# Kernel optimization log

Hardware: AMD Instinct MI355X
Metric: run time of the kernel (lower is better)

Reference implementation:

```python
import jax, jax.numpy as jnp
import numpy as np

N_NODES = 100000
N_EDGES = 3200000
IN_DIM = 4
BIG = 32
HID = 2
BN_EPS = 1e-5


def _lin_init(key, fan_in, fan_out):
    k1, k2 = jax.random.split(key)
    bound = 1.0 / np.sqrt(fan_in)
    W = jax.random.uniform(k1, (fan_in, fan_out), minval=-bound, maxval=bound, dtype=jnp.float32)
    b = jax.random.uniform(k2, (fan_out,), minval=-bound, maxval=bound, dtype=jnp.float32)
    return W, b


def setup_inputs() -> dict:
    key = jax.random.key(0)
    ks = jax.random.split(key, 12)
    x = jax.random.normal(ks[0], (N_NODES, IN_DIM), dtype=jnp.float32)
    edge_index = jax.random.randint(ks[1], (2, N_EDGES), 0, N_NODES, dtype=jnp.int32)
    eps_noise = jax.random.normal(ks[2], (N_NODES, HID), dtype=jnp.float32)
    # batchnorm affine params
    bn_gamma = jnp.ones((IN_DIM,), jnp.float32)
    bn_beta = jnp.zeros((IN_DIM,), jnp.float32)
    # encoder EdgeConv MLP: 2*IN_DIM -> BIG -> BIG
    eW1, eb1 = _lin_init(ks[3], 2 * IN_DIM, BIG)
    eW2, eb2 = _lin_init(ks[4], BIG, BIG)
    # mu / logvar heads
    mW, mb = _lin_init(ks[5], BIG, HID)
    vW, vb = _lin_init(ks[6], BIG, HID)
    # decoder EdgeConv MLP: 2*HID -> BIG -> BIG -> IN_DIM
    dW1, db1 = _lin_init(ks[7], 2 * HID, BIG)
    dW2, db2 = _lin_init(ks[8], BIG, BIG)
    dW3, db3 = _lin_init(ks[9], BIG, IN_DIM)
    return dict(x=x, edge_index=edge_index, eps_noise=eps_noise,
                bn_gamma=bn_gamma, bn_beta=bn_beta,
                eW1=eW1, eb1=eb1, eW2=eW2, eb2=eb2,
                mW=mW, mb=mb, vW=vW, vb=vb,
                dW1=dW1, db1=db1, dW2=dW2, db2=db2, dW3=dW3, db3=db3)


def _segment_mean(msgs, tgt, n):
    s = jax.ops.segment_sum(msgs, tgt, num_segments=n)
    c = jax.ops.segment_sum(jnp.ones((msgs.shape[0],), msgs.dtype), tgt, num_segments=n)
    return s / jnp.maximum(c, 1.0)[:, None]


def _edge_conv(x, edge_index, mlp):
    # PyG EdgeConv: h_i = mean_{j->i} nn([x_i, x_j - x_i])
    src, tgt = edge_index[0], edge_index[1]
    x_i = x[tgt]                      # [E, F]
    x_j = x[src]                      # [E, F]
    feat = jnp.concatenate([x_i, x_j - x_i], axis=-1)  # [E, 2F]
    msg = mlp(feat)                   # [E, F_out]
    return _segment_mean(msg, tgt, x.shape[0])


def reference(x, edge_index, eps_noise, bn_gamma, bn_beta,
              eW1, eb1, eW2, eb2, mW, mb, vW, vb,
              dW1, db1, dW2, db2, dW3, db3):
    # BatchNorm1d (training mode: batch statistics, biased variance)
    mean = jnp.mean(x, axis=0)
    var = jnp.var(x, axis=0)
    xn = (x - mean) * jax.lax.rsqrt(var + BN_EPS) * bn_gamma + bn_beta

    enc_mlp = lambda f: jax.nn.relu(jax.nn.relu(f @ eW1 + eb1) @ eW2 + eb2)
    h = _edge_conv(xn, edge_index, enc_mlp)           # [N, BIG]

    mu = h @ mW + mb                                  # [N, HID]
    log_var = h @ vW + vb                             # [N, HID]
    z = mu + eps_noise * jnp.exp(0.5 * log_var)       # reparameterize

    dec_mlp = lambda f: jax.nn.relu(jax.nn.relu(f @ dW1 + db1) @ dW2 + db2) @ dW3 + db3
    out = _edge_conv(z, edge_index, dec_mlp)          # [N, IN_DIM]
    return out, mu, log_var
```

## Files before the change

### kernel.cpp

```cpp
#include <hip/hip_runtime.h>
#include <math.h>

#define N_NODES 100000
#define N_EDGES 3200000
#define NBLK_EDGE ((N_EDGES + 255) / 256)
#define NBLK_NODE ((N_NODES + 255) / 256)

#define NB 64
#define NBUCK ((N_NODES + NB - 1) / NB)
#define NSLICE 256
#define SLICE (N_EDGES / NSLICE)
#define P2 2048

typedef _Float16 h2f16 __attribute__((ext_vector_type(2)));
typedef __fp16 f16x8 __attribute__((ext_vector_type(8)));
typedef float f32x4 __attribute__((ext_vector_type(4)));
typedef unsigned u32x4 __attribute__((ext_vector_type(4)));

#define PK_ENC_A2 0
#define PK_DEC_A2 512
#define PK_ENC_W1 1024
#define PK_DEC_W1 1152
#define PK_ENC_H 1216
#define PK_DEC_H 1280
#define PK_TOTAL 1344

__device__ __forceinline__ h2f16 mkh2(float a, float b) {
  h2f16 h;
  h.x = (_Float16)a;
  h.y = (_Float16)b;
  return h;
}
__device__ __forceinline__ float fdot2(h2f16 a, h2f16 b, float c) {
  return __builtin_amdgcn_fdot2(a, b, c, false);
}
__device__ __forceinline__ h2f16 pk(float a, float b) {
  auto r = __builtin_amdgcn_cvt_pkrtz(a, b);
  return __builtin_bit_cast(h2f16, r);
}
__device__ __forceinline__ unsigned h2u(h2f16 h) {
  return __builtin_bit_cast(unsigned, h);
}
__device__ __forceinline__ f32x4 mfma16(f16x8 a, f16x8 b, f32x4 c) {
  return __builtin_amdgcn_mfma_f32_16x16x32_f16(a, b, c, 0, 0, 0);
}

__global__ __launch_bounds__(256) void pack_weights(
    const float* __restrict__ eW1, const float* __restrict__ eW2,
    const float* __restrict__ mW, const float* __restrict__ vW,
    const float* __restrict__ dW1, const float* __restrict__ dW2,
    const float* __restrict__ dW3, h2f16* __restrict__ wpk) {
  int t = threadIdx.x;
  for (int i = t; i < 512; i += 256) {
    int tl = i >> 8, rest = i & 255, lane = rest >> 2, p = rest & 3;
    int q = lane >> 4, c = lane & 15;
    int k0 = q * 8 + 2 * p, out = 16 * tl + c;
    wpk[PK_ENC_A2 + i] = mkh2(eW2[k0 * 32 + out], eW2[(k0 + 1) * 32 + out]);
    wpk[PK_DEC_A2 + i] = mkh2(dW2[k0 * 32 + out], dW2[(k0 + 1) * 32 + out]);
  }
  for (int i = t; i < 128; i += 256) {
    int q = i >> 5, j = (i >> 2) & 7, kp = i & 3;
    wpk[PK_ENC_W1 + i] =
        mkh2(eW1[(2 * kp) * 32 + q * 8 + j], eW1[(2 * kp + 1) * 32 + q * 8 + j]);
  }
  for (int i = t; i < 64; i += 256) {
    int q = i >> 4, j = (i >> 1) & 7, kp = i & 1;
    wpk[PK_DEC_W1 + i] =
        mkh2(dW1[(2 * kp) * 32 + q * 8 + j], dW1[(2 * kp + 1) * 32 + q * 8 + j]);
  }
  for (int i = t; i < 64; i += 256) {
    int q = i >> 4, r = (i >> 2) & 3, h = i & 3;
    int o0 = 4 * q + r, o1 = 16 + 4 * q + r;
    float w0 = (h < 2) ? mW[o0 * 2 + h] : vW[o0 * 2 + (h - 2)];
    float w1 = (h < 2) ? mW[o1 * 2 + h] : vW[o1 * 2 + (h - 2)];
    wpk[PK_ENC_H + i] = mkh2(w0, w1);
    wpk[PK_DEC_H + i] = mkh2(dW3[o0 * 4 + h], dW3[o1 * 4 + h]);
  }
}

__global__ void bn_reduce(const float4* __restrict__ x, float* __restrict__ bns) {
  float s0 = 0, s1 = 0, s2 = 0, s3 = 0, q0 = 0, q1 = 0, q2 = 0, q3 = 0;
  for (int i = blockIdx.x * blockDim.x + threadIdx.x; i < N_NODES;
       i += gridDim.x * blockDim.x) {
    float4 v = x[i];
    s0 += v.x; s1 += v.y; s2 += v.z; s3 += v.w;
    q0 += v.x * v.x; q1 += v.y * v.y; q2 += v.z * v.z; q3 += v.w * v.w;
  }
#pragma unroll
  for (int o = 32; o; o >>= 1) {
    s0 += __shfl_down(s0, o); s1 += __shfl_down(s1, o);
    s2 += __shfl_down(s2, o); s3 += __shfl_down(s3, o);
    q0 += __shfl_down(q0, o); q1 += __shfl_down(q1, o);
    q2 += __shfl_down(q2, o); q3 += __shfl_down(q3, o);
  }
  __shared__ float red[4][8];
  int w = threadIdx.x >> 6;
  if ((threadIdx.x & 63) == 0) {
    red[w][0] = s0; red[w][1] = s1; red[w][2] = s2; red[w][3] = s3;
    red[w][4] = q0; red[w][5] = q1; red[w][6] = q2; red[w][7] = q3;
  }
  __syncthreads();
  if (threadIdx.x < 8) {
    float acc = red[0][threadIdx.x] + red[1][threadIdx.x] +
                red[2][threadIdx.x] + red[3][threadIdx.x];
    atomicAdd(&bns[threadIdx.x], acc);
  }
}

__global__ void bn_final(const float* __restrict__ bns,
                         const float* __restrict__ gamma,
                         const float* __restrict__ beta,
                         float* __restrict__ ab) {
  int d = threadIdx.x;
  if (d < 4) {
    float mean = bns[d] * (1.0f / N_NODES);
    float var = bns[4 + d] * (1.0f / N_NODES) - mean * mean;
    float a = gamma[d] * rsqrtf(var + 1e-5f);
    ab[d] = a;
    ab[4 + d] = beta[d] - mean * a;
  }
}

__global__ __launch_bounds__(256) void edge_hist(const int* __restrict__ tgt,
                                                 unsigned* __restrict__ hist) {
  __shared__ unsigned h[NBUCK];
  for (int i = threadIdx.x; i < NBUCK; i += 256) h[i] = 0;
  __syncthreads();
  int e0 = blockIdx.x * SLICE;
  for (int i = threadIdx.x; i < SLICE; i += 256)
    atomicAdd(&h[((unsigned)tgt[e0 + i]) >> 6], 1u);
  __syncthreads();
  for (int i = threadIdx.x; i < NBUCK; i += 256)
    hist[(size_t)blockIdx.x * NBUCK + i] = h[i];
}

__global__ __launch_bounds__(256) void bucket_tot(const unsigned* __restrict__ hist,
                                                  unsigned* __restrict__ tot) {
  int k = blockIdx.x * 256 + threadIdx.x;
  if (k >= NBUCK) return;
  unsigned s = 0;
#pragma unroll 8
  for (int b = 0; b < NSLICE; ++b) s += hist[(size_t)b * NBUCK + k];
  tot[k] = s;
}

__global__ __launch_bounds__(1024) void bucket_start(const unsigned* __restrict__ tot,
                                                     unsigned* __restrict__ start) {
  __shared__ unsigned sa[P2], sb[P2];
  for (int k = threadIdx.x; k < P2; k += 1024)
    sa[k] = (k < NBUCK) ? tot[k] : 0u;
  __syncthreads();
  unsigned *srcp = sa, *dstp = sb;
  for (int off = 1; off < P2; off <<= 1) {
    for (int k = threadIdx.x; k < P2; k += 1024)
      dstp[k] = srcp[k] + (k >= off ? srcp[k - off] : 0u);
    __syncthreads();
    unsigned* t = srcp; srcp = dstp; dstp = t;
  }
  for (int k = threadIdx.x; k <= NBUCK; k += 1024)
    start[k] = (k == 0) ? 0u : srcp[k - 1];
}

__global__ __launch_bounds__(256) void bucket_bases(unsigned* __restrict__ hist,
                                                    const unsigned* __restrict__ start) {
  int wv = threadIdx.x >> 6, lane = threadIdx.x & 63;
  int k = blockIdx.x * 4 + wv;
  if (k >= NBUCK) return;
  unsigned v0 = hist[(size_t)(4 * lane + 0) * NBUCK + k];
  unsigned v1 = hist[(size_t)(4 * lane + 1) * NBUCK + k];
  unsigned v2 = hist[(size_t)(4 * lane + 2) * NBUCK + k];
  unsigned v3 = hist[(size_t)(4 * lane + 3) * NBUCK + k];
  unsigned p1 = v0, p2 = v0 + v1, p3 = v0 + v1 + v2;
  unsigned s = p3 + v3;
  unsigned incl = s;
#pragma unroll
  for (int off = 1; off < 64; off <<= 1) {
    unsigned t = __shfl_up(incl, off);
    incl += (lane >= off) ? t : 0u;
  }
  unsigned base = start[k] + (incl - s);
  hist[(size_t)(4 * lane + 0) * NBUCK + k] = base;
  hist[(size_t)(4 * lane + 1) * NBUCK + k] = base + p1;
  hist[(size_t)(4 * lane + 2) * NBUCK + k] = base + p2;
  hist[(size_t)(4 * lane + 3) * NBUCK + k] = base + p3;
}

__global__ __launch_bounds__(256) void edge_place(
    const int* __restrict__ src, const int* __restrict__ tgt,
    const unsigned* __restrict__ hist, const unsigned* __restrict__ start,
    unsigned* __restrict__ payload) {
  __shared__ unsigned stage[SLICE];
  __shared__ unsigned offA[NBUCK];
  __shared__ unsigned A2[NBUCK];
  int s = blockIdx.x, tid = threadIdx.x;
  for (int k = tid; k < NBUCK; k += 256) {
    unsigned gb = hist[(size_t)s * NBUCK + k];
    unsigned nb = (s == NSLICE - 1) ? start[k + 1]
                                    : hist[(size_t)(s + 1) * NBUCK + k];
    offA[k] = gb;
    A2[k] = nb - gb;
  }
  __syncthreads();
  for (int d = 1; d < NBUCK; d <<= 1) {
    unsigned tmp[7];
    int m = 0;
    for (int k = tid; k < NBUCK; k += 256, ++m)
      tmp[m] = (k >= d) ? A2[k - d] : 0u;
    __syncthreads();
    m = 0;
    for (int k = tid; k < NBUCK; k += 256, ++m) A2[k] += tmp[m];
    __syncthreads();
  }
  {
    unsigned tmp[7];
    int m = 0;
    for (int k = tid; k < NBUCK; k += 256, ++m)
      tmp[m] = (k == 0) ? 0u : A2[k - 1];
    __syncthreads();
    m = 0;
    for (int k = tid; k < NBUCK; k += 256, ++m) {
      offA[k] -= tmp[m];
      A2[k] = tmp[m];
    }
    __syncthreads();
  }
  int e0 = s * SLICE;
  for (int i = tid; i < SLICE; i += 256) {
    unsigned t = (unsigned)tgt[e0 + i];
    unsigned sr = (unsigned)src[e0 + i];
    unsigned b = t >> 6;
    unsigned lp = atomicAdd(&A2[b], 1u);
    stage[lp] = sr | ((t & 63u) << 17);
  }
  __syncthreads();
  for (int b = tid; b < NBUCK; b += 256) {
    unsigned beg = (b == 0) ? 0u : A2[b - 1];
    unsigned end = A2[b];
    unsigned go = offA[b];
    for (unsigned i = beg; i < end; ++i) payload[go + i] = stage[i];
  }
}

__global__ __launch_bounds__(256) void enc_bucket(
    const float4* __restrict__ x, const unsigned* __restrict__ payload,
    const unsigned* __restrict__ start, const float* __restrict__ ab,
    const float* __restrict__ eb1, const float* __restrict__ eb2,
    const h2f16* __restrict__ wpk, float2* __restrict__ mpart,
    float2* __restrict__ vpart, float* __restrict__ cpart) {
  __shared__ float aM0[NB], aM1[NB], aV0[NB], aV1[NB], aC[NB];
  __shared__ float4 xt[NB];
  int k = blockIdx.x, node0 = k * NB, h = blockIdx.y;
  int tid = threadIdx.x, w = tid >> 6, lane = tid & 63;
  int q = lane >> 4, c = lane & 15;
  if (tid < NB) {
    int n = node0 + tid;
    aM0[tid] = 0; aM1[tid] = 0; aV0[tid] = 0; aV1[tid] = 0; aC[tid] = 0;
    xt[tid] = x[n < N_NODES ? n : 0];
  }
  __syncthreads();
  float a0 = ab[0], a1 = ab[1], a2 = ab[2], a3 = ab[3];
  float b0 = ab[4], b1 = ab[5], b2 = ab[6], b3 = ab[7];
  const u32x4* a2b = (const u32x4*)(wpk + PK_ENC_A2);
  f16x8 A0 = __builtin_bit_cast(f16x8, a2b[lane]);
  f16x8 A1 = __builtin_bit_cast(f16x8, a2b[64 + lane]);
  h2f16 w1e[32];
#pragma unroll
  for (int i = 0; i < 32; ++i) w1e[i] = wpk[PK_ENC_W1 + q * 32 + i];
  h2f16 hw[16];
#pragma unroll
  for (int i = 0; i < 16; ++i) hw[i] = wpk[PK_ENC_H + q * 16 + i];
  float eb1v[8];
#pragma unroll
  for (int j = 0; j < 8; ++j) eb1v[j] = eb1[q * 8 + j];
  float e2a[4], e2b[4];
#pragma unroll
  for (int r = 0; r < 4; ++r) {
    e2a[r] = eb2[4 * q + r];
    e2b[r] = eb2[16 + 4 * q + r];
  }
  unsigned s0v = start[k], s1v = start[k + 1];
  unsigned len = s1v - s0v, halfv = (len + 1) >> 1;
  unsigned lo = s0v + (h ? halfv : 0u);
  unsigned hi = h ? s1v : (s0v + halfv);
  for (unsigned base = lo + (unsigned)w * 32; base < hi; base += 128) {
    unsigned eA = base + (unsigned)c;
    unsigned eB = eA + 16;
    unsigned pA = payload[eA < hi ? eA : hi - 1];
    unsigned pB = payload[eB < hi ? eB : hi - 1];
    int siA = (int)(pA & 0x1FFFFu), siB = (int)(pB & 0x1FFFFu);
    int ltiA = (int)(pA >> 17), ltiB = (int)(pB >> 17);
    float4 xjA = x[siA];
    float4 xjB = x[siB];
    float4 xiA = xt[ltiA];
    float4 xiB = xt[ltiB];
    h2f16 fA0 = pk(fmaf(a0, xiA.x, b0), fmaf(a1, xiA.y, b1));
    h2f16 fA1 = pk(fmaf(a2, xiA.z, b2), fmaf(a3, xiA.w, b3));
    h2f16 fA2 = pk(a0 * (xjA.x - xiA.x), a1 * (xjA.y - xiA.y));
    h2f16 fA3 = pk(a2 * (xjA.z - xiA.z), a3 * (xjA.w - xiA.w));
    h2f16 fB0 = pk(fmaf(a0, xiB.x, b0), fmaf(a1, xiB.y, b1));
    h2f16 fB1 = pk(fmaf(a2, xiB.z, b2), fmaf(a3, xiB.w, b3));
    h2f16 fB2 = pk(a0 * (xjB.x - xiB.x), a1 * (xjB.y - xiB.y));
    h2f16 fB3 = pk(a2 * (xjB.z - xiB.z), a3 * (xjB.w - xiB.w));
    float rA[8], rB[8];
#pragma unroll
    for (int j = 0; j < 8; ++j) {
      float uA = eb1v[j], uB = eb1v[j];
      uA = fdot2(fA0, w1e[4 * j + 0], uA);
      uB = fdot2(fB0, w1e[4 * j + 0], uB);
      uA = fdot2(fA1, w1e[4 * j + 1], uA);
      uB = fdot2(fB1, w1e[4 * j + 1], uB);
      uA = fdot2(fA2, w1e[4 * j + 2], uA);
      uB = fdot2(fB2, w1e[4 * j + 2], uB);
      uA = fdot2(fA3, w1e[4 * j + 3], uA);
      uB = fdot2(fB3, w1e[4 * j + 3], uB);
      rA[j] = fmaxf(uA, 0.0f);
      rB[j] = fmaxf(uB, 0.0f);
    }
    u32x4 buA, buB;
    buA[0] = h2u(pk(rA[0], rA[1])); buA[1] = h2u(pk(rA[2], rA[3]));
    buA[2] = h2u(pk(rA[4], rA[5])); buA[3] = h2u(pk(rA[6], rA[7]));
    buB[0] = h2u(pk(rB[0], rB[1])); buB[1] = h2u(pk(rB[2], rB[3]));
    buB[2] = h2u(pk(rB[4], rB[5])); buB[3] = h2u(pk(rB[6], rB[7]));
    f16x8 BA = __builtin_bit_cast(f16x8, buA);
    f16x8 BB = __builtin_bit_cast(f16x8, buB);
    f32x4 zf = {0.f, 0.f, 0.f, 0.f};
    f32x4 C0A = mfma16(A0, BA, zf), C1A = mfma16(A1, BA, zf);
    f32x4 C0B = mfma16(A0, BB, zf), C1B = mfma16(A1, BB, zf);
    float m0A = 0, m1A = 0, v0A = 0, v1A = 0;
    float m0B = 0, m1B = 0, v0B = 0, v1B = 0;
#pragma unroll
    for (int rr = 0; rr < 4; ++rr) {
      h2f16 hA = pk(fmaxf(C0A[rr] + e2a[rr], 0.0f),
                    fmaxf(C1A[rr] + e2b[rr], 0.0f));
      h2f16 hB = pk(fmaxf(C0B[rr] + e2a[rr], 0.0f),
                    fmaxf(C1B[rr] + e2b[rr], 0.0f));
      m0A = fdot2(hA, hw[4 * rr + 0], m0A);
      m0B = fdot2(hB, hw[4 * rr + 0], m0B);
      m1A = fdot2(hA, hw[4 * rr + 1], m1A);
      m1B = fdot2(hB, hw[4 * rr + 1], m1B);
      v0A = fdot2(hA, hw[4 * rr + 2], v0A);
      v0B = fdot2(hB, hw[4 * rr + 2], v0B);
      v1A = fdot2(hA, hw[4 * rr + 3], v1A);
      v1B = fdot2(hB, hw[4 * rr + 3], v1B);
    }
    m0A += __shfl_xor(m0A, 16); m0A += __shfl_xor(m0A, 32);
    m1A += __shfl_xor(m1A, 16); m1A += __shfl_xor(m1A, 32);
    v0A += __shfl_xor(v0A, 16); v0A += __shfl_xor(v0A, 32);
    v1A += __shfl_xor(v1A, 16); v1A += __shfl_xor(v1A, 32);
    m0B += __shfl_xor(m0B, 16); m0B += __shfl_xor(m0B, 32);
    m1B += __shfl_xor(m1B, 16); m1B += __shfl_xor(m1B, 32);
    v0B += __shfl_xor(v0B, 16); v0B += __shfl_xor(v0B, 32);
    v1B += __shfl_xor(v1B, 16); v1B += __shfl_xor(v1B, 32);
    if (lane < 16) {
      if (eA < hi) {
        atomicAdd(&aM0[ltiA], m0A);
        atomicAdd(&aM1[ltiA], m1A);
        atomicAdd(&aV0[ltiA], v0A);
        atomicAdd(&aV1[ltiA], v1A);
        atomicAdd(&aC[ltiA], 1.0f);
      }
      if (eB < hi) {
        atomicAdd(&aM0[ltiB], m0B);
        atomicAdd(&aM1[ltiB], m1B);
        atomicAdd(&aV0[ltiB], v0B);
        atomicAdd(&aV1[ltiB], v1B);
        atomicAdd(&aC[ltiB], 1.0f);
      }
    }
  }
  __syncthreads();
  if (tid < NB) {
    int n = node0 + tid;
    if (n < N_NODES) {
      mpart[(size_t)h * N_NODES + n] = make_float2(aM0[tid], aM1[tid]);
      vpart[(size_t)h * N_NODES + n] = make_float2(aV0[tid], aV1[tid]);
      cpart[(size_t)h * N_NODES + n] = aC[tid];
    }
  }
}

__global__ __launch_bounds__(256) void node_mid(
    const float2* __restrict__ mpart, const float2* __restrict__ vpart,
    const float* __restrict__ cpart, const float* __restrict__ eps2,
    const float* __restrict__ mbias, const float* __restrict__ vbias,
    float* __restrict__ z, float* __restrict__ cntC,
    float2* __restrict__ muOut, float2* __restrict__ lvOut) {
  int n = blockIdx.x * 256 + threadIdx.x;
  if (n >= N_NODES) return;
  float2 ma = mpart[n], mb2 = mpart[N_NODES + n];
  float2 va = vpart[n], vb2 = vpart[N_NODES + n];
  float cc = cpart[n] + cpart[N_NODES + n];
  float inv = 1.0f / fmaxf(cc, 1.0f);
  float mu0 = fmaf(ma.x + mb2.x, inv, mbias[0]);
  float mu1 = fmaf(ma.y + mb2.y, inv, mbias[1]);
  float lv0 = fmaf(va.x + vb2.x, inv, vbias[0]);
  float lv1 = fmaf(va.y + vb2.y, inv, vbias[1]);
  cntC[n] = cc;
  muOut[n] = make_float2(mu0, mu1);
  lvOut[n] = make_float2(lv0, lv1);
  z[2 * n + 0] = fmaf(eps2[2 * n + 0], expf(0.5f * lv0), mu0);
  z[2 * n + 1] = fmaf(eps2[2 * n + 1], expf(0.5f * lv1), mu1);
}

__global__ __launch_bounds__(256) void dec_bucket(
    const float2* __restrict__ z, const unsigned* __restrict__ payload,
    const unsigned* __restrict__ start, const float* __restrict__ db1,
    const float* __restrict__ db2, const float* __restrict__ db3,
    const h2f16* __restrict__ wpk, float4* __restrict__ opart) {
  __shared__ float aO0[NB], aO1[NB], aO2[NB], aO3[NB];
  __shared__ float2 zt[NB];
  int k = blockIdx.x, node0 = k * NB, h = blockIdx.y;
  int tid = threadIdx.x, w = tid >> 6, lane = tid & 63;
  int q = lane >> 4, c = lane & 15;
  if (tid < NB) {
    int n = node0 + tid;
    aO0[tid] = 0; aO1[tid] = 0; aO2[tid] = 0; aO3[tid] = 0;
    zt[tid] = z[n < N_NODES ? n : 0];
  }
  __syncthreads();
  const u32x4* a2b = (const u32x4*)(wpk + PK_DEC_A2);
  f16x8 A0 = __builtin_bit_cast(f16x8, a2b[lane]);
  f16x8 A1 = __builtin_bit_cast(f16x8, a2b[64 + lane]);
  h2f16 w1d[16];
#pragma unroll
  for (int i = 0; i < 16; ++i) w1d[i] = wpk[PK_DEC_W1 + q * 16 + i];
  h2f16 hw[16];
#pragma unroll
  for (int i = 0; i < 16; ++i) hw[i] = wpk[PK_DEC_H + q * 16 + i];
  float db1v[8];
#pragma unroll
  for (int j = 0; j < 8; ++j) db1v[j] = db1[q * 8 + j];
  float d2a[4], d2b[4];
#pragma unroll
  for (int r = 0; r < 4; ++r) {
    d2a[r] = db2[4 * q + r];
    d2b[r] = db2[16 + 4 * q + r];
  }
  float b3_0 = db3[0], b3_1 = db3[1], b3_2 = db3[2], b3_3 = db3[3];
  unsigned s0v = start[k], s1v = start[k + 1];
  unsigned len = s1v - s0v, halfv = (len + 1) >> 1;
  unsigned lo = s0v + (h ? halfv : 0u);
  unsigned hi = h ? s1v : (s0v + halfv);
  for (unsigned base = lo + (unsigned)w * 32; base < hi; base += 128) {
    unsigned eA = base + (unsigned)c;
    unsigned eB = eA + 16;
    unsigned pA = payload[eA < hi ? eA : hi - 1];
    unsigned pB = payload[eB < hi ? eB : hi - 1];
    int siA = (int)(pA & 0x1FFFFu), siB = (int)(pB & 0x1FFFFu);
    int ltiA = (int)(pA >> 17), ltiB = (int)(pB >> 17);
    float2 zjA = z[siA];
    float2 zjB = z[siB];
    float2 ziA = zt[ltiA];
    float2 ziB = zt[ltiB];
    h2f16 fA0 = pk(ziA.x, ziA.y);
    h2f16 fA1 = pk(zjA.x - ziA.x, zjA.y - ziA.y);
    h2f16 fB0 = pk(ziB.x, ziB.y);
    h2f16 fB1 = pk(zjB.x - ziB.x, zjB.y - ziB.y);
    float rA[8], rB[8];
#pragma unroll
    for (int j = 0; j < 8; ++j) {
      float uA = db1v[j], uB = db1v[j];
      uA = fdot2(fA0, w1d[2 * j + 0], uA);
      uB = fdot2(fB0, w1d[2 * j + 0], uB);
      uA = fdot2(fA1, w1d[2 * j + 1], uA);
      uB = fdot2(fB1, w1d[2 * j + 1], uB);
      rA[j] = fmaxf(uA, 0.0f);
      rB[j] = fmaxf(uB, 0.0f);
    }
    u32x4 buA, buB;
    buA[0] = h2u(pk(rA[0], rA[1])); buA[1] = h2u(pk(rA[2], rA[3]));
    buA[2] = h2u(pk(rA[4], rA[5])); buA[3] = h2u(pk(rA[6], rA[7]));
    buB[0] = h2u(pk(rB[0], rB[1])); buB[1] = h2u(pk(rB[2], rB[3]));
    buB[2] = h2u(pk(rB[4], rB[5])); buB[3] = h2u(pk(rB[6], rB[7]));
    f16x8 BA = __builtin_bit_cast(f16x8, buA);
    f16x8 BB = __builtin_bit_cast(f16x8, buB);
    f32x4 zf = {0.f, 0.f, 0.f, 0.f};
    f32x4 C0A = mfma16(A0, BA, zf), C1A = mfma16(A1, BA, zf);
    f32x4 C0B = mfma16(A0, BB, zf), C1B = mfma16(A1, BB, zf);
    float o0A = 0, o1A = 0, o2A = 0, o3A = 0;
    float o0B = 0, o1B = 0, o2B = 0, o3B = 0;
#pragma unroll
    for (int rr = 0; rr < 4; ++rr) {
      h2f16 hA = pk(fmaxf(C0A[rr] + d2a[rr], 0.0f),
                    fmaxf(C1A[rr] + d2b[rr], 0.0f));
      h2f16 hB = pk(fmaxf(C0B[rr] + d2a[rr], 0.0f),
                    fmaxf(C1B[rr] + d2b[rr], 0.0f));
      o0A = fdot2(hA, hw[4 * rr + 0], o0A);
      o0B = fdot2(hB, hw[4 * rr + 0], o0B);
      o1A = fdot2(hA, hw[4 * rr + 1], o1A);
      o1B = fdot2(hB, hw[4 * rr + 1], o1B);
      o2A = fdot2(hA, hw[4 * rr + 2], o2A);
      o2B = fdot2(hB, hw[4 * rr + 2], o2B);
      o3A = fdot2(hA, hw[4 * rr + 3], o3A);
      o3B = fdot2(hB, hw[4 * rr + 3], o3B);
    }
    o0A += __shfl_xor(o0A, 16); o0A += __shfl_xor(o0A, 32);
    o1A += __shfl_xor(o1A, 16); o1A += __shfl_xor(o1A, 32);
    o2A += __shfl_xor(o2A, 16); o2A += __shfl_xor(o2A, 32);
    o3A += __shfl_xor(o3A, 16); o3A += __shfl_xor(o3A, 32);
    o0B += __shfl_xor(o0B, 16); o0B += __shfl_xor(o0B, 32);
    o1B += __shfl_xor(o1B, 16); o1B += __shfl_xor(o1B, 32);
    o2B += __shfl_xor(o2B, 16); o2B += __shfl_xor(o2B, 32);
    o3B += __shfl_xor(o3B, 16); o3B += __shfl_xor(o3B, 32);
    if (lane < 16) {
      if (eA < hi) {
        atomicAdd(&aO0[ltiA], o0A + b3_0);
        atomicAdd(&aO1[ltiA], o1A + b3_1);
        atomicAdd(&aO2[ltiA], o2A + b3_2);
        atomicAdd(&aO3[ltiA], o3A + b3_3);
      }
      if (eB < hi) {
        atomicAdd(&aO0[ltiB], o0B + b3_0);
        atomicAdd(&aO1[ltiB], o1B + b3_1);
        atomicAdd(&aO2[ltiB], o2B + b3_2);
        atomicAdd(&aO3[ltiB], o3B + b3_3);
      }
    }
  }
  __syncthreads();
  if (tid < NB) {
    int n = node0 + tid;
    if (n < N_NODES)
      opart[(size_t)h * N_NODES + n] =
          make_float4(aO0[tid], aO1[tid], aO2[tid], aO3[tid]);
  }
}

__global__ __launch_bounds__(256) void node_final(
    const float4* __restrict__ opart, const float* __restrict__ cntC,
    float4* __restrict__ outp) {
  int n = blockIdx.x * 256 + threadIdx.x;
  if (n >= N_NODES) return;
  float4 a = opart[n], b = opart[N_NODES + n];
  float inv = 1.0f / fmaxf(cntC[n], 1.0f);
  outp[n] = make_float4((a.x + b.x) * inv, (a.y + b.y) * inv,
                        (a.z + b.z) * inv, (a.w + b.w) * inv);
}

__device__ __forceinline__ void atomAddF(float* p, float v) {
  unsafeAtomicAdd(p, v);
}

__global__ __launch_bounds__(256) void enc_edge_fb(
    const float4* __restrict__ x, const int* __restrict__ esrc,
    const int* __restrict__ etgt, const float* __restrict__ ab,
    const float* __restrict__ eW1, const float* __restrict__ eb1,
    const float* __restrict__ eW2, const float* __restrict__ eb2,
    const float* __restrict__ mW, const float* __restrict__ vW,
    float* __restrict__ msum, float* __restrict__ vsum,
    float* __restrict__ cnt) {
  int e = blockIdx.x * 256 + threadIdx.x;
  if (e >= N_EDGES) return;
  int si = esrc[e], ti = etgt[e];
  float4 xi = x[ti];
  float4 xj = x[si];
  float a0 = ab[0], a1 = ab[1], a2 = ab[2], a3 = ab[3];
  float b0 = ab[4], b1 = ab[5], b2 = ab[6], b3 = ab[7];
  float feat[8];
  feat[0] = fmaf(a0, xi.x, b0);
  feat[1] = fmaf(a1, xi.y, b1);
  feat[2] = fmaf(a2, xi.z, b2);
  feat[3] = fmaf(a3, xi.w, b3);
  feat[4] = a0 * (xj.x - xi.x);
  feat[5] = a1 * (xj.y - xi.y);
  feat[6] = a2 * (xj.z - xi.z);
  feat[7] = a3 * (xj.w - xi.w);
  float h1[32];
#pragma unroll 8
  for (int j = 0; j < 32; ++j) {
    float acc = eb1[j];
#pragma unroll
    for (int kk = 0; kk < 8; ++kk) acc = fmaf(feat[kk], eW1[kk * 32 + j], acc);
    h1[j] = fmaxf(acc, 0.0f);
  }
  float m0 = 0, m1 = 0, v0 = 0, v1 = 0;
#pragma unroll 4
  for (int j = 0; j < 32; ++j) {
    float acc = eb2[j];
#pragma unroll
    for (int kk = 0; kk < 32; ++kk) acc = fmaf(h1[kk], eW2[kk * 32 + j], acc);
    float h2 = fmaxf(acc, 0.0f);
    m0 = fmaf(h2, mW[j * 2 + 0], m0);
    m1 = fmaf(h2, mW[j * 2 + 1], m1);
    v0 = fmaf(h2, vW[j * 2 + 0], v0);
    v1 = fmaf(h2, vW[j * 2 + 1], v1);
  }
  atomAddF(&msum[ti * 2 + 0], m0);
  atomAddF(&msum[ti * 2 + 1], m1);
  atomAddF(&vsum[ti * 2 + 0], v0);
  atomAddF(&vsum[ti * 2 + 1], v1);
  atomAddF(&cnt[ti], 1.0f);
}

__global__ __launch_bounds__(256) void dec_edge_fb(
    const float2* __restrict__ z, const int* __restrict__ esrc,
    const int* __restrict__ etgt, const float* __restrict__ dW1,
    const float* __restrict__ db1, const float* __restrict__ dW2,
    const float* __restrict__ db2, const float* __restrict__ dW3,
    const float* __restrict__ db3, float* __restrict__ osum) {
  int e = blockIdx.x * 256 + threadIdx.x;
  if (e >= N_EDGES) return;
  int si = esrc[e], ti = etgt[e];
  float2 zi = z[ti], zj = z[si];
  float f0 = zi.x, f1 = zi.y, f2 = zj.x - zi.x, f3 = zj.y - zi.y;
  float h1[32];
#pragma unroll 8
  for (int j = 0; j < 32; ++j) {
    float acc = db1[j];
    acc = fmaf(f0, dW1[0 * 32 + j], acc);
    acc = fmaf(f1, dW1[1 * 32 + j], acc);
    acc = fmaf(f2, dW1[2 * 32 + j], acc);
    acc = fmaf(f3, dW1[3 * 32 + j], acc);
    h1[j] = fmaxf(acc, 0.0f);
  }
  float o0 = db3[0], o1 = db3[1], o2 = db3[2], o3 = db3[3];
#pragma unroll 4
  for (int j = 0; j < 32; ++j) {
    float acc = db2[j];
#pragma unroll
    for (int kk = 0; kk < 32; ++kk) acc = fmaf(h1[kk], dW2[kk * 32 + j], acc);
    float h2 = fmaxf(acc, 0.0f);
    o0 = fmaf(h2, dW3[j * 4 + 0], o0);
    o1 = fmaf(h2, dW3[j * 4 + 1], o1);
    o2 = fmaf(h2, dW3[j * 4 + 2], o2);
    o3 = fmaf(h2, dW3[j * 4 + 3], o3);
  }
  atomAddF(&osum[4 * ti + 0], o0);
  atomAddF(&osum[4 * ti + 1], o1);
  atomAddF(&osum[4 * ti + 2], o2);
  atomAddF(&osum[4 * ti + 3], o3);
}

__global__ __launch_bounds__(256) void node_mid_fb(
    float* __restrict__ msum, float* __restrict__ vsum,
    const float* __restrict__ cnt, const float* __restrict__ eps2,
    const float* __restrict__ mb, const float* __restrict__ vb,
    float* __restrict__ z) {
  int n = blockIdx.x * 256 + threadIdx.x;
  if (n >= N_NODES) return;
  float inv = 1.0f / fmaxf(cnt[n], 1.0f);
  float mu0 = fmaf(msum[2 * n + 0], inv, mb[0]);
  float mu1 = fmaf(msum[2 * n + 1], inv, mb[1]);
  float lv0 = fmaf(vsum[2 * n + 0], inv, vb[0]);
  float lv1 = fmaf(vsum[2 * n + 1], inv, vb[1]);
  msum[2 * n + 0] = mu0;
  msum[2 * n + 1] = mu1;
  vsum[2 * n + 0] = lv0;
  vsum[2 * n + 1] = lv1;
  z[2 * n + 0] = fmaf(eps2[2 * n + 0], expf(0.5f * lv0), mu0);
  z[2 * n + 1] = fmaf(eps2[2 * n + 1], expf(0.5f * lv1), mu1);
}

__global__ __launch_bounds__(256) void node_final_fb(
    float* __restrict__ osum, const float* __restrict__ cnt) {
  int n = blockIdx.x * 256 + threadIdx.x;
  if (n >= N_NODES) return;
  float inv = 1.0f / fmaxf(cnt[n], 1.0f);
  float4* o4 = (float4*)osum;
  float4 v = o4[n];
  v.x *= inv; v.y *= inv; v.z *= inv; v.w *= inv;
  o4[n] = v;
}

extern "C" void kernel_launch(void* const* d_in, const int* in_sizes, int n_in,
                              void* d_out, int out_size, void* d_ws,
                              size_t ws_size, hipStream_t stream) {
  const float* x = (const float*)d_in[0];
  const int* ei = (const int*)d_in[1];
  const float* eps = (const float*)d_in[2];
  const float* bng = (const float*)d_in[3];
  const float* bnb = (const float*)d_in[4];
  const float* eW1 = (const float*)d_in[5];
  const float* eb1 = (const float*)d_in[6];
  const float* eW2 = (const float*)d_in[7];
  const float* eb2 = (const float*)d_in[8];
  const float* mW = (const float*)d_in[9];
  const float* mb = (const float*)d_in[10];
  const float* vW = (const float*)d_in[11];
  const float* vb = (const float*)d_in[12];
  const float* dW1 = (const float*)d_in[13];
  const float* db1 = (const float*)d_in[14];
  const float* dW2 = (const float*)d_in[15];
  const float* db2 = (const float*)d_in[16];
  const float* dW3 = (const float*)d_in[17];
  const float* db3 = (const float*)d_in[18];

  float* out = (float*)d_out;
  const size_t N = N_NODES;

  float* wsf = (float*)d_ws;
  float* bns = wsf;
  float* ab = wsf + 8;
  float* z = wsf + 16;
  float* cntC = z + 2 * N;
  float* cpart = cntC + N;
  float2* mpart = (float2*)(cpart + 2 * N);
  float2* vpart = mpart + 2 * N;
  float4* opart = (float4*)((float*)vpart + 4 * N);
  unsigned* start = (unsigned*)((float*)opart + 8 * N);
  unsigned* hist = start + (NBUCK + 1);
  unsigned* payload = hist + (size_t)NSLICE * NBUCK;
  h2f16* wpk = (h2f16*)(payload + N_EDGES);
  const size_t REQ = (16 + 21 * N) * sizeof(float) +
                     ((size_t)(NBUCK + 1) + (size_t)NSLICE * NBUCK + N_EDGES +
                      PK_TOTAL) *
                         sizeof(unsigned);

  if (ws_size >= REQ) {
    (void)hipMemsetAsync(bns, 0, 8 * sizeof(float), stream);
    pack_weights<<<1, 256, 0, stream>>>(eW1, eW2, mW, vW, dW1, dW2, dW3, wpk);
    bn_reduce<<<256, 256, 0, stream>>>((const float4*)x, bns);
    bn_final<<<1, 64, 0, stream>>>(bns, bng, bnb, ab);
    edge_hist<<<NSLICE, 256, 0, stream>>>(ei + N_EDGES, hist);
    bucket_tot<<<(NBUCK + 255) / 256, 256, 0, stream>>>(hist, payload);
    bucket_start<<<1, 1024, 0, stream>>>(payload, start);
    bucket_bases<<<(NBUCK + 3) / 4, 256, 0, stream>>>(hist, start);
    edge_place<<<NSLICE, 256, 0, stream>>>(ei, ei + N_EDGES, hist, start,
                                           payload);
    dim3 gE(NBUCK, 2);
    enc_bucket<<<gE, 256, 0, stream>>>((const float4*)x, payload, start, ab,
                                       eb1, eb2, wpk, mpart, vpart, cpart);
    node_mid<<<NBLK_NODE, 256, 0, stream>>>(mpart, vpart, cpart, eps, mb, vb,
                                            z, cntC, (float2*)(out + 4 * N),
                                            (float2*)(out + 6 * N));
    dec_bucket<<<gE, 256, 0, stream>>>((const float2*)z, payload, start, db1,
                                       db2, db3, wpk, opart);
    node_final<<<NBLK_NODE, 256, 0, stream>>>(opart, cntC, (float4*)out);
  } else {
    float* cntf = wsf + 16;
    float* zf = wsf + 16 + N;
    float* msum = out + 4 * N;
    float* vsum = out + 6 * N;
    (void)hipMemsetAsync(d_out, 0, 8 * N * sizeof(float), stream);
    (void)hipMemsetAsync(d_ws, 0, (16 + N) * sizeof(float), stream);
    bn_reduce<<<256, 256, 0, stream>>>((const float4*)x, bns);
    bn_final<<<1, 64, 0, stream>>>(bns, bng, bnb, ab);
    enc_edge_fb<<<NBLK_EDGE, 256, 0, stream>>>((const float4*)x, ei,
                                               ei + N_EDGES, ab, eW1, eb1, eW2,
                                               eb2, mW, vW, msum, vsum, cntf);
    node_mid_fb<<<NBLK_NODE, 256, 0, stream>>>(msum, vsum, cntf, eps, mb, vb,
                                               zf);
    dec_edge_fb<<<NBLK_EDGE, 256, 0, stream>>>((const float2*)zf, ei,
                                               ei + N_EDGES, dW1, db1, dW2, db2,
                                               dW3, db3, out);
    node_final_fb<<<NBLK_NODE, 256, 0, stream>>>(out, cntf);
  }
}
```

Measured before the change: 404.8 us.

## Split first EdgeConv layer into per-node target and source projections

The first linear layer of each EdgeConv MLP is factored as W1·[x_i, x_j-x_i] = (W1a-W1b)·x_i + W1b·x_j. A per-node fp16 source projection Q (32 halves per node) is precomputed in a new enc_prep kernel and in node_mid, and each bucket block computes the target part for its 64 nodes into shared memory. Per-edge work drops to a gather plus packed half add+ReLU in place of 8/16 fdot2 operations, but each edge now gathers 64 bytes per source instead of 16 or 8, which raises random-access memory traffic. The workspace is reorganised so hist aliases Q and opart aliases mpart, and fp16 rounding of the partial sums happens earlier.

```diff
diff --git a/kernel.cpp b/kernel.cpp
--- a/kernel.cpp
+++ b/kernel.cpp
@@ -19,11 +19,9 @@
 
 #define PK_ENC_A2 0
 #define PK_DEC_A2 512
-#define PK_ENC_W1 1024
-#define PK_DEC_W1 1152
-#define PK_ENC_H 1216
-#define PK_DEC_H 1280
-#define PK_TOTAL 1344
+#define PK_ENC_H 1024
+#define PK_DEC_H 1088
+#define PK_TOTAL 1152
 
 __device__ __forceinline__ h2f16 mkh2(float a, float b) {
   h2f16 h;
@@ -41,14 +39,24 @@
 __device__ __forceinline__ unsigned h2u(h2f16 h) {
   return __builtin_bit_cast(unsigned, h);
 }
+__device__ __forceinline__ unsigned pku(float a, float b) {
+  return h2u(pk(a, b));
+}
 __device__ __forceinline__ f32x4 mfma16(f16x8 a, f16x8 b, f32x4 c) {
   return __builtin_amdgcn_mfma_f32_16x16x32_f16(a, b, c, 0, 0, 0);
 }
+__device__ __forceinline__ unsigned addrelu2(unsigned p, unsigned q) {
+  h2f16 a = __builtin_bit_cast(h2f16, p);
+  h2f16 b = __builtin_bit_cast(h2f16, q);
+  h2f16 s = a + b;
+  h2f16 zero = {(_Float16)0.0f, (_Float16)0.0f};
+  h2f16 r = __builtin_elementwise_max(s, zero);
+  return __builtin_bit_cast(unsigned, r);
+}
 
 __global__ __launch_bounds__(256) void pack_weights(
-    const float* __restrict__ eW1, const float* __restrict__ eW2,
-    const float* __restrict__ mW, const float* __restrict__ vW,
-    const float* __restrict__ dW1, const float* __restrict__ dW2,
+    const float* __restrict__ eW2, const float* __restrict__ mW,
+    const float* __restrict__ vW, const float* __restrict__ dW2,
     const float* __restrict__ dW3, h2f16* __restrict__ wpk) {
   int t = threadIdx.x;
   for (int i = t; i < 512; i += 256) {
@@ -57,16 +65,6 @@
     int k0 = q * 8 + 2 * p, out = 16 * tl + c;
     wpk[PK_ENC_A2 + i] = mkh2(eW2[k0 * 32 + out], eW2[(k0 + 1) * 32 + out]);
     wpk[PK_DEC_A2 + i] = mkh2(dW2[k0 * 32 + out], dW2[(k0 + 1) * 32 + out]);
-  }
-  for (int i = t; i < 128; i += 256) {
-    int q = i >> 5, j = (i >> 2) & 7, kp = i & 3;
-    wpk[PK_ENC_W1 + i] =
-        mkh2(eW1[(2 * kp) * 32 + q * 8 + j], eW1[(2 * kp + 1) * 32 + q * 8 + j]);
-  }
-  for (int i = t; i < 64; i += 256) {
-    int q = i >> 4, j = (i >> 1) & 7, kp = i & 1;
-    wpk[PK_DEC_W1 + i] =
-        mkh2(dW1[(2 * kp) * 32 + q * 8 + j], dW1[(2 * kp + 1) * 32 + q * 8 + j]);
   }
   for (int i = t; i < 64; i += 256) {
     int q = i >> 4, r = (i >> 2) & 3, h = i & 3;
@@ -241,14 +239,45 @@
   }
 }
 
+__global__ __launch_bounds__(256) void enc_prep(
+    const float4* __restrict__ x, const float* __restrict__ ab,
+    const float* __restrict__ eW1, u32x4* __restrict__ Q) {
+  int n = blockIdx.x * 256 + threadIdx.x;
+  if (n >= N_NODES) return;
+  float4 v = x[n];
+  float xn0 = fmaf(ab[0], v.x, ab[4]);
+  float xn1 = fmaf(ab[1], v.y, ab[5]);
+  float xn2 = fmaf(ab[2], v.z, ab[6]);
+  float xn3 = fmaf(ab[3], v.w, ab[7]);
+  unsigned qp[16];
+#pragma unroll 4
+  for (int p = 0; p < 16; ++p) {
+    int o0 = 2 * p, o1 = 2 * p + 1;
+    float u0 = xn0 * eW1[4 * 32 + o0] + xn1 * eW1[5 * 32 + o0] +
+               xn2 * eW1[6 * 32 + o0] + xn3 * eW1[7 * 32 + o0];
+    float u1 = xn0 * eW1[4 * 32 + o1] + xn1 * eW1[5 * 32 + o1] +
+               xn2 * eW1[6 * 32 + o1] + xn3 * eW1[7 * 32 + o1];
+    qp[p] = pku(u0, u1);
+  }
+#pragma unroll
+  for (int r = 0; r < 4; ++r) {
+    u32x4 o;
+    o[0] = qp[4 * r]; o[1] = qp[4 * r + 1];
+    o[2] = qp[4 * r + 2]; o[3] = qp[4 * r + 3];
+    Q[n * 4 + r] = o;
+  }
+}
+
 __global__ __launch_bounds__(256) void enc_bucket(
     const float4* __restrict__ x, const unsigned* __restrict__ payload,
     const unsigned* __restrict__ start, const float* __restrict__ ab,
-    const float* __restrict__ eb1, const float* __restrict__ eb2,
+    const float* __restrict__ eW1, const float* __restrict__ eb1,
+    const float* __restrict__ eb2, const u32x4* __restrict__ Q,
     const h2f16* __restrict__ wpk, float2* __restrict__ mpart,
     float2* __restrict__ vpart, float* __restrict__ cpart) {
   __shared__ float aM0[NB], aM1[NB], aV0[NB], aV1[NB], aC[NB];
   __shared__ float4 xt[NB];
+  __shared__ u32x4 Pl[NB * 4];
   int k = blockIdx.x, node0 = k * NB, h = blockIdx.y;
   int tid = threadIdx.x, w = tid >> 6, lane = tid & 63;
   int q = lane >> 4, c = lane & 15;
@@ -258,20 +287,36 @@
     xt[tid] = x[n < N_NODES ? n : 0];
   }
   __syncthreads();
-  float a0 = ab[0], a1 = ab[1], a2 = ab[2], a3 = ab[3];
-  float b0 = ab[4], b1 = ab[5], b2 = ab[6], b3 = ab[7];
+  {
+    int s = tid >> 6, n = tid & 63;
+    float4 v = xt[n];
+    float xn0 = fmaf(ab[0], v.x, ab[4]);
+    float xn1 = fmaf(ab[1], v.y, ab[5]);
+    float xn2 = fmaf(ab[2], v.z, ab[6]);
+    float xn3 = fmaf(ab[3], v.w, ab[7]);
+    u32x4 o;
+#pragma unroll
+    for (int jp = 0; jp < 4; ++jp) {
+      int o0 = s * 8 + 2 * jp, o1 = o0 + 1;
+      float u0 = eb1[o0] + xn0 * (eW1[0 * 32 + o0] - eW1[4 * 32 + o0]) +
+                 xn1 * (eW1[1 * 32 + o0] - eW1[5 * 32 + o0]) +
+                 xn2 * (eW1[2 * 32 + o0] - eW1[6 * 32 + o0]) +
+                 xn3 * (eW1[3 * 32 + o0] - eW1[7 * 32 + o0]);
+      float u1 = eb1[o1] + xn0 * (eW1[0 * 32 + o1] - eW1[4 * 32 + o1]) +
+                 xn1 * (eW1[1 * 32 + o1] - eW1[5 * 32 + o1]) +
+                 xn2 * (eW1[2 * 32 + o1] - eW1[6 * 32 + o1]) +
+                 xn3 * (eW1[3 * 32 + o1] - eW1[7 * 32 + o1]);
+      o[jp] = pku(u0, u1);
+    }
+    Pl[n * 4 + s] = o;
+  }
+  __syncthreads();
   const u32x4* a2b = (const u32x4*)(wpk + PK_ENC_A2);
   f16x8 A0 = __builtin_bit_cast(f16x8, a2b[lane]);
   f16x8 A1 = __builtin_bit_cast(f16x8, a2b[64 + lane]);
-  h2f16 w1e[32];
-#pragma unroll
-  for (int i = 0; i < 32; ++i) w1e[i] = wpk[PK_ENC_W1 + q * 32 + i];
   h2f16 hw[16];
 #pragma unroll
   for (int i = 0; i < 16; ++i) hw[i] = wpk[PK_ENC_H + q * 16 + i];
-  float eb1v[8];
-#pragma unroll
-  for (int j = 0; j < 8; ++j) eb1v[j] = eb1[q * 8 + j];
   float e2a[4], e2b[4];
 #pragma unroll
   for (int r = 0; r < 4; ++r) {
@@ -289,38 +334,16 @@
     unsigned pB = payload[eB < hi ? eB : hi - 1];
     int siA = (int)(pA & 0x1FFFFu), siB = (int)(pB & 0x1FFFFu);
     int ltiA = (int)(pA >> 17), ltiB = (int)(pB >> 17);
-    float4 xjA = x[siA];
-    float4 xjB = x[siB];
-    float4 xiA = xt[ltiA];
-    float4 xiB = xt[ltiB];
-    h2f16 fA0 = pk(fmaf(a0, xiA.x, b0), fmaf(a1, xiA.y, b1));
-    h2f16 fA1 = pk(fmaf(a2, xiA.z, b2), fmaf(a3, xiA.w, b3));
-    h2f16 fA2 = pk(a0 * (xjA.x - xiA.x), a1 * (xjA.y - xiA.y));
-    h2f16 fA3 = pk(a2 * (xjA.z - xiA.z), a3 * (xjA.w - xiA.w));
-    h2f16 fB0 = pk(fmaf(a0, xiB.x, b0), fmaf(a1, xiB.y, b1));
-    h2f16 fB1 = pk(fmaf(a2, xiB.z, b2), fmaf(a3, xiB.w, b3));
-    h2f16 fB2 = pk(a0 * (xjB.x - xiB.x), a1 * (xjB.y - xiB.y));
-    h2f16 fB3 = pk(a2 * (xjB.z - xiB.z), a3 * (xjB.w - xiB.w));
-    float rA[8], rB[8];
-#pragma unroll
-    for (int j = 0; j < 8; ++j) {
-      float uA = eb1v[j], uB = eb1v[j];
-      uA = fdot2(fA0, w1e[4 * j + 0], uA);
-      uB = fdot2(fB0, w1e[4 * j + 0], uB);
-      uA = fdot2(fA1, w1e[4 * j + 1], uA);
-      uB = fdot2(fB1, w1e[4 * j + 1], uB);
-      uA = fdot2(fA2, w1e[4 * j + 2], uA);
-      uB = fdot2(fB2, w1e[4 * j + 2], uB);
-      uA = fdot2(fA3, w1e[4 * j + 3], uA);
-      uB = fdot2(fB3, w1e[4 * j + 3], uB);
-      rA[j] = fmaxf(uA, 0.0f);
-      rB[j] = fmaxf(uB, 0.0f);
-    }
+    u32x4 qA = Q[siA * 4 + q];
+    u32x4 qB = Q[siB * 4 + q];
+    u32x4 pLA = Pl[ltiA * 4 + q];
+    u32x4 pLB = Pl[ltiB * 4 + q];
     u32x4 buA, buB;
-    buA[0] = h2u(pk(rA[0], rA[1])); buA[1] = h2u(pk(rA[2], rA[3]));
-    buA[2] = h2u(pk(rA[4], rA[5])); buA[3] = h2u(pk(rA[6], rA[7]));
-    buB[0] = h2u(pk(rB[0], rB[1])); buB[1] = h2u(pk(rB[2], rB[3]));
-    buB[2] = h2u(pk(rB[4], rB[5])); buB[3] = h2u(pk(rB[6], rB[7]));
+#pragma unroll
+    for (int i = 0; i < 4; ++i) {
+      buA[i] = addrelu2(pLA[i], qA[i]);
+      buB[i] = addrelu2(pLB[i], qB[i]);
+    }
     f16x8 BA = __builtin_bit_cast(f16x8, buA);
     f16x8 BB = __builtin_bit_cast(f16x8, buB);
     f32x4 zf = {0.f, 0.f, 0.f, 0.f};
@@ -383,8 +406,9 @@
     const float2* __restrict__ mpart, const float2* __restrict__ vpart,
     const float* __restrict__ cpart, const float* __restrict__ eps2,
     const float* __restrict__ mbias, const float* __restrict__ vbias,
-    float* __restrict__ z, float* __restrict__ cntC,
-    float2* __restrict__ muOut, float2* __restrict__ lvOut) {
+    const float* __restrict__ dW1, float* __restrict__ z,
+    float* __restrict__ cntC, float2* __restrict__ muOut,
+    float2* __restrict__ lvOut, u32x4* __restrict__ Qd) {
   int n = blockIdx.x * 256 + threadIdx.x;
   if (n >= N_NODES) return;
   float2 ma = mpart[n], mb2 = mpart[N_NODES + n];
@@ -398,17 +422,36 @@
   cntC[n] = cc;
   muOut[n] = make_float2(mu0, mu1);
   lvOut[n] = make_float2(lv0, lv1);
-  z[2 * n + 0] = fmaf(eps2[2 * n + 0], expf(0.5f * lv0), mu0);
-  z[2 * n + 1] = fmaf(eps2[2 * n + 1], expf(0.5f * lv1), mu1);
+  float z0 = fmaf(eps2[2 * n + 0], expf(0.5f * lv0), mu0);
+  float z1 = fmaf(eps2[2 * n + 1], expf(0.5f * lv1), mu1);
+  z[2 * n + 0] = z0;
+  z[2 * n + 1] = z1;
+  unsigned qp[16];
+#pragma unroll 4
+  for (int p = 0; p < 16; ++p) {
+    int o0 = 2 * p, o1 = 2 * p + 1;
+    float u0 = z0 * dW1[2 * 32 + o0] + z1 * dW1[3 * 32 + o0];
+    float u1 = z0 * dW1[2 * 32 + o1] + z1 * dW1[3 * 32 + o1];
+    qp[p] = pku(u0, u1);
+  }
+#pragma unroll
+  for (int r = 0; r < 4; ++r) {
+    u32x4 o;
+    o[0] = qp[4 * r]; o[1] = qp[4 * r + 1];
+    o[2] = qp[4 * r + 2]; o[3] = qp[4 * r + 3];
+    Qd[n * 4 + r] = o;
+  }
 }
 
 __global__ __launch_bounds__(256) void dec_bucket(
     const float2* __restrict__ z, const unsigned* __restrict__ payload,
-    const unsigned* __restrict__ start, const float* __restrict__ db1,
-    const float* __restrict__ db2, const float* __restrict__ db3,
+    const unsigned* __restrict__ start, const float* __restrict__ dW1,
+    const float* __restrict__ db1, const float* __restrict__ db2,
+    const float* __restrict__ db3, const u32x4* __restrict__ Q,
     const h2f16* __restrict__ wpk, float4* __restrict__ opart) {
   __shared__ float aO0[NB], aO1[NB], aO2[NB], aO3[NB];
   __shared__ float2 zt[NB];
+  __shared__ u32x4 Pl[NB * 4];
   int k = blockIdx.x, node0 = k * NB, h = blockIdx.y;
   int tid = threadIdx.x, w = tid >> 6, lane = tid & 63;
   int q = lane >> 4, c = lane & 15;
@@ -418,18 +461,28 @@
     zt[tid] = z[n < N_NODES ? n : 0];
   }
   __syncthreads();
+  {
+    int s = tid >> 6, n = tid & 63;
+    float2 v = zt[n];
+    u32x4 o;
+#pragma unroll
+    for (int jp = 0; jp < 4; ++jp) {
+      int o0 = s * 8 + 2 * jp, o1 = o0 + 1;
+      float u0 = db1[o0] + v.x * (dW1[0 * 32 + o0] - dW1[2 * 32 + o0]) +
+                 v.y * (dW1[1 * 32 + o0] - dW1[3 * 32 + o0]);
+      float u1 = db1[o1] + v.x * (dW1[0 * 32 + o1] - dW1[2 * 32 + o1]) +
+                 v.y * (dW1[1 * 32 + o1] - dW1[3 * 32 + o1]);
+      o[jp] = pku(u0, u1);
+    }
+    Pl[n * 4 + s] = o;
+  }
+  __syncthreads();
   const u32x4* a2b = (const u32x4*)(wpk + PK_DEC_A2);
   f16x8 A0 = __builtin_bit_cast(f16x8, a2b[lane]);
   f16x8 A1 = __builtin_bit_cast(f16x8, a2b[64 + lane]);
-  h2f16 w1d[16];
-#pragma unroll
-  for (int i = 0; i < 16; ++i) w1d[i] = wpk[PK_DEC_W1 + q * 16 + i];
   h2f16 hw[16];
 #pragma unroll
   for (int i = 0; i < 16; ++i) hw[i] = wpk[PK_DEC_H + q * 16 + i];
-  float db1v[8];
-#pragma unroll
-  for (int j = 0; j < 8; ++j) db1v[j] = db1[q * 8 + j];
   float d2a[4], d2b[4];
 #pragma unroll
   for (int r = 0; r < 4; ++r) {
@@ -448,30 +501,16 @@
     unsigned pB = payload[eB < hi ? eB : hi - 1];
     int siA = (int)(pA & 0x1FFFFu), siB = (int)(pB & 0x1FFFFu);
     int ltiA = (int)(pA >> 17), ltiB = (int)(pB >> 17);
-    float2 zjA = z[siA];
-    float2 zjB = z[siB];
-    float2 ziA = zt[ltiA];
-    float2 ziB = zt[ltiB];
-    h2f16 fA0 = pk(ziA.x, ziA.y);
-    h2f16 fA1 = pk(zjA.x - ziA.x, zjA.y - ziA.y);
-    h2f16 fB0 = pk(ziB.x, ziB.y);
-    h2f16 fB1 = pk(zjB.x - ziB.x, zjB.y - ziB.y);
-    float rA[8], rB[8];
-#pragma unroll
-    for (int j = 0; j < 8; ++j) {
-      float uA = db1v[j], uB = db1v[j];
-      uA = fdot2(fA0, w1d[2 * j + 0], uA);
-      uB = fdot2(fB0, w1d[2 * j + 0], uB);
-      uA = fdot2(fA1, w1d[2 * j + 1], uA);
-      uB = fdot2(fB1, w1d[2 * j + 1], uB);
-      rA[j] = fmaxf(uA, 0.0f);
-      rB[j] = fmaxf(uB, 0.0f);
-    }
+    u32x4 qA = Q[siA * 4 + q];
+    u32x4 qB = Q[siB * 4 + q];
+    u32x4 pLA = Pl[ltiA * 4 + q];
+    u32x4 pLB = Pl[ltiB * 4 + q];
     u32x4 buA, buB;
-    buA[0] = h2u(pk(rA[0], rA[1])); buA[1] = h2u(pk(rA[2], rA[3]));
-    buA[2] = h2u(pk(rA[4], rA[5])); buA[3] = h2u(pk(rA[6], rA[7]));
-    buB[0] = h2u(pk(rB[0], rB[1])); buB[1] = h2u(pk(rB[2], rB[3]));
-    buB[2] = h2u(pk(rB[4], rB[5])); buB[3] = h2u(pk(rB[6], rB[7]));
+#pragma unroll
+    for (int i = 0; i < 4; ++i) {
+      buA[i] = addrelu2(pLA[i], qA[i]);
+      buB[i] = addrelu2(pLB[i], qB[i]);
+    }
     f16x8 BA = __builtin_bit_cast(f16x8, buA);
     f16x8 BB = __builtin_bit_cast(f16x8, buB);
     f32x4 zf = {0.f, 0.f, 0.f, 0.f};
@@ -696,19 +735,23 @@
   float* cpart = cntC + N;
   float2* mpart = (float2*)(cpart + 2 * N);
   float2* vpart = mpart + 2 * N;
-  float4* opart = (float4*)((float*)vpart + 4 * N);
-  unsigned* start = (unsigned*)((float*)opart + 8 * N);
-  unsigned* hist = start + (NBUCK + 1);
-  unsigned* payload = hist + (size_t)NSLICE * NBUCK;
+  float4* opart = (float4*)mpart;
+  unsigned* start = (unsigned*)((float*)vpart + 4 * N);
+  unsigned* payload = start + (NBUCK + 1);
   h2f16* wpk = (h2f16*)(payload + N_EDGES);
-  const size_t REQ = (16 + 21 * N) * sizeof(float) +
-                     ((size_t)(NBUCK + 1) + (size_t)NSLICE * NBUCK + N_EDGES +
-                      PK_TOTAL) *
+  unsigned* qh = (unsigned*)(wpk + PK_TOTAL);
+  unsigned* hist = qh;
+  u32x4* Q = (u32x4*)qh;
+  const size_t QH = (size_t)N * 16 > (size_t)NSLICE * NBUCK
+                        ? (size_t)N * 16
+                        : (size_t)NSLICE * NBUCK;
+  const size_t REQ = (16 + 13 * N) * sizeof(float) +
+                     ((size_t)(NBUCK + 1) + N_EDGES + PK_TOTAL + QH) *
                          sizeof(unsigned);
 
   if (ws_size >= REQ) {
     (void)hipMemsetAsync(bns, 0, 8 * sizeof(float), stream);
-    pack_weights<<<1, 256, 0, stream>>>(eW1, eW2, mW, vW, dW1, dW2, dW3, wpk);
+    pack_weights<<<1, 256, 0, stream>>>(eW2, mW, vW, dW2, dW3, wpk);
     bn_reduce<<<256, 256, 0, stream>>>((const float4*)x, bns);
     bn_final<<<1, 64, 0, stream>>>(bns, bng, bnb, ab);
     edge_hist<<<NSLICE, 256, 0, stream>>>(ei + N_EDGES, hist);
@@ -717,14 +760,17 @@
     bucket_bases<<<(NBUCK + 3) / 4, 256, 0, stream>>>(hist, start);
     edge_place<<<NSLICE, 256, 0, stream>>>(ei, ei + N_EDGES, hist, start,
                                            payload);
+    enc_prep<<<NBLK_NODE, 256, 0, stream>>>((const float4*)x, ab, eW1, Q);
     dim3 gE(NBUCK, 2);
     enc_bucket<<<gE, 256, 0, stream>>>((const float4*)x, payload, start, ab,
-                                       eb1, eb2, wpk, mpart, vpart, cpart);
+                                       eW1, eb1, eb2, Q, wpk, mpart, vpart,
+                                       cpart);
     node_mid<<<NBLK_NODE, 256, 0, stream>>>(mpart, vpart, cpart, eps, mb, vb,
-                                            z, cntC, (float2*)(out + 4 * N),
-                                            (float2*)(out + 6 * N));
-    dec_bucket<<<gE, 256, 0, stream>>>((const float2*)z, payload, start, db1,
-                                       db2, db3, wpk, opart);
+                                            dW1, z, cntC,
+                                            (float2*)(out + 4 * N),
+                                            (float2*)(out + 6 * N), Q);
+    dec_bucket<<<gE, 256, 0, stream>>>((const float2*)z, payload, start, dW1,
+                                       db1, db2, db3, Q, wpk, opart);
     node_final<<<NBLK_NODE, 256, 0, stream>>>(opart, cntC, (float4*)out);
   } else {
     float* cntf = wsf + 16;
```

New measurement: 423.6 us. +4.7%, slower.
